# Performance work log

Measured on AMD Instinct MI355X. Metric: run time of the kernel, lower is better.

Reference implementation:

```python
import jax, jax.numpy as jnp
import numpy as np

HEADS = 16
HIDDEN = 1024
DH = HIDDEN // HEADS
EPS = 1e-6


def setup_inputs() -> dict:
    key = jax.random.key(0)
    ks = jax.random.split(key, 18)
    B, S, D, H = 8, 4096, HIDDEN, HEADS
    std = 0.02
    inp = {
        "x": jax.random.normal(ks[0], (B, S, D), dtype=jnp.float32),
        "mask": jnp.zeros((B, 1, S), dtype=jnp.float32),
        "Wq": std * jax.random.normal(ks[1], (D, D), dtype=jnp.float32),
        "bq": jnp.zeros((D,), jnp.float32),
        "Wk": std * jax.random.normal(ks[2], (D, D), dtype=jnp.float32),
        "bk": jnp.zeros((D,), jnp.float32),
        "Wv": std * jax.random.normal(ks[3], (D, D), dtype=jnp.float32),
        "bv": jnp.zeros((D,), jnp.float32),
        "Wa": std * jax.random.normal(ks[4], (D, H), dtype=jnp.float32),
        "ba": jnp.zeros((H,), jnp.float32),
        "Wb": std * jax.random.normal(ks[5], (D, H), dtype=jnp.float32),
        "bb": jnp.zeros((H,), jnp.float32),
        "Wu": std * jax.random.normal(ks[6], (D, D), dtype=jnp.float32),
        "bu": jnp.zeros((D,), jnp.float32),
        "Wo": std * jax.random.normal(ks[7], (D, D), dtype=jnp.float32),
        "bo": jnp.zeros((D,), jnp.float32),
        "ln_g": jnp.ones((D,), jnp.float32),
        "ln_b": jnp.zeros((D,), jnp.float32),
    }
    return inp


def reference(x, mask, Wq, bq, Wk, bk, Wv, bv, Wa, ba, Wb, bb, Wu, bu, Wo, bo, ln_g, ln_b):
    B, S, D = x.shape
    H, dh = HEADS, D // HEADS
    scale = (D / H) ** -0.5

    q = x @ Wq + bq  # [B,S,D]
    k = x @ Wk + bk
    v = x @ Wv + bv

    # alpha pooling of q
    ascore = jnp.swapaxes((q @ Wa + ba) * scale, 1, 2) + mask  # [B,H,S]
    aw = jax.nn.softmax(ascore, axis=-1)
    qh = q.reshape(B, S, H, dh)
    q_av = jnp.einsum("bhs,bshd->bhd", aw, qh).reshape(B, 1, D)  # global query

    p = k * q_av  # [B,S,D], broadcast over seq

    # beta pooling of p
    bscore = jnp.swapaxes((p @ Wb + bb) * scale, 1, 2) + mask  # [B,H,S]
    bw = jax.nn.softmax(bscore, axis=-1)
    ph = p.reshape(B, S, H, dh)
    p_av = jnp.einsum("bhs,bshd->bhd", bw, ph).reshape(B, 1, D)  # global key

    u = p_av * v  # [B,S,D]
    r = u @ Wu + bu
    attn_out = (r + q) @ Wo + bo

    y = x + attn_out  # residual (dropout is identity at inference)
    mu = jnp.mean(y, axis=-1, keepdims=True)
    var = jnp.mean(jnp.square(y - mu), axis=-1, keepdims=True)
    return (y - mu) * jax.lax.rsqrt(var + EPS) * ln_g + ln_b
```

## Files before the change

### kernel.cpp

```cpp
#include <hip/hip_runtime.h>

typedef unsigned short u16;
typedef __bf16 bf16x8 __attribute__((ext_vector_type(8)));
typedef float  f32x4  __attribute__((ext_vector_type(4)));

__device__ __forceinline__ float b2f(u16 u) {
    unsigned int v = ((unsigned int)u) << 16;
    return __builtin_bit_cast(float, v);
}
__device__ __forceinline__ u16 f2b(float f) {
    unsigned int v = __builtin_bit_cast(unsigned int, f);
    v += 0x7fffu + ((v >> 16) & 1u);
    return (u16)(v >> 16);
}

#define GLD16(gp, lp) __builtin_amdgcn_global_load_lds( \
    (const __attribute__((address_space(1))) void*)(gp), \
    (__attribute__((address_space(3))) void*)(lp), 16, 0, 0)


__global__ __launch_bounds__(256) void convert_x(const float* __restrict__ x,
                                                 u16* __restrict__ xb) {
    size_t i = ((size_t)blockIdx.x * 256 + threadIdx.x) * 8;
    float4 v0 = *(const float4*)(x + i);
    float4 v1 = *(const float4*)(x + i + 4);
    ushort4 o0, o1;
    o0.x = f2b(v0.x); o0.y = f2b(v0.y); o0.z = f2b(v0.z); o0.w = f2b(v0.w);
    o1.x = f2b(v1.x); o1.y = f2b(v1.y); o1.z = f2b(v1.z); o1.w = f2b(v1.w);
    *(ushort4*)(xb + i)     = o0;
    *(ushort4*)(xb + i + 4) = o1;
}

__global__ __launch_bounds__(256) void transpose_w(const float* __restrict__ W,
                                                   u16* __restrict__ Wt) {
    __shared__ float tile[64][65];
    int kt = (blockIdx.x & 15) * 64;
    int nt = (blockIdx.x >> 4) * 64;
    int tid = threadIdx.x;
    int r = tid >> 4, c4 = (tid & 15) * 4;
    #pragma unroll
    for (int p = 0; p < 4; ++p) {
        int k = kt + p * 16 + r;
        float4 v = *(const float4*)(W + (size_t)k * 1024 + nt + c4);
        tile[c4 + 0][p * 16 + r] = v.x;
        tile[c4 + 1][p * 16 + r] = v.y;
        tile[c4 + 2][p * 16 + r] = v.z;
        tile[c4 + 3][p * 16 + r] = v.w;
    }
    __syncthreads();
    #pragma unroll
    for (int p = 0; p < 4; ++p) {
        int nl = p * 16 + r;
        ushort4 o;
        o.x = f2b(tile[nl][c4 + 0]); o.y = f2b(tile[nl][c4 + 1]);
        o.z = f2b(tile[nl][c4 + 2]); o.w = f2b(tile[nl][c4 + 3]);
        *(ushort4*)(Wt + (size_t)(nt + nl) * 1024 + kt + c4) = o;
    }
}

__global__ __launch_bounds__(256) void wu_prime(const float* __restrict__ Wu,
                                                const float* __restrict__ p_av,
                                                u16* __restrict__ Wut) {
    __shared__ float tile[64][65];
    int kt = (blockIdx.x & 15) * 64;
    int nt = (blockIdx.x >> 4) * 64;
    int tid = threadIdx.x;
    int r = tid >> 4, c4 = (tid & 15) * 4;
    #pragma unroll
    for (int p = 0; p < 4; ++p) {
        int k = kt + p * 16 + r;
        float4 v = *(const float4*)(Wu + (size_t)k * 1024 + nt + c4);
        tile[c4 + 0][p * 16 + r] = v.x;
        tile[c4 + 1][p * 16 + r] = v.y;
        tile[c4 + 2][p * 16 + r] = v.z;
        tile[c4 + 3][p * 16 + r] = v.w;
    }
    __syncthreads();
    for (int b = 0; b < 8; ++b) {
        float4 pv = *(const float4*)(p_av + (size_t)b * 1024 + kt + c4);
        #pragma unroll
        for (int p = 0; p < 4; ++p) {
            int nl = p * 16 + r;
            ushort4 o;
            o.x = f2b(tile[nl][c4 + 0] * pv.x);
            o.y = f2b(tile[nl][c4 + 1] * pv.y);
            o.z = f2b(tile[nl][c4 + 2] * pv.z);
            o.w = f2b(tile[nl][c4 + 3] * pv.w);
            *(ushort4*)(Wut + ((size_t)b * 1024 + nt + nl) * 1024 + kt + c4) = o;
        }
    }
}

__global__ __launch_bounds__(256) void wat_prep(const float* __restrict__ Wa,
                                                u16* __restrict__ Wat) {
    int idx = blockIdx.x * 256 + threadIdx.x;
    int h = idx >> 10, k = idx & 1023;
    Wat[idx] = f2b(Wa[(k << 4) + h]);
}

__global__ __launch_bounds__(256) void wbt_prep(const float* __restrict__ Wb,
                                                const float* __restrict__ q_av,
                                                u16* __restrict__ Wbt) {
    int idx = blockIdx.x * 256 + threadIdx.x;
    int b = idx >> 14, rem = idx & 16383;
    int h = rem >> 10, k = rem & 1023;
    Wbt[idx] = f2b(Wb[(k << 4) + h] * q_av[(b << 10) + k]);
}

__global__ __launch_bounds__(256) void bias_concat(const float* __restrict__ bq,
                                                   const float* __restrict__ bk,
                                                   const float* __restrict__ bv,
                                                   float* __restrict__ outb) {
    int i = blockIdx.x * 256 + threadIdx.x;
    outb[i] = (i < 1024) ? bq[i] : (i < 2048 ? bk[i - 1024] : bv[i - 2048]);
}

__global__ __launch_bounds__(512, 2)
void gemm_bf16(const u16* __restrict__ A, int lda,
               const u16* __restrict__ Bt,
               const float* __restrict__ bias,
               const u16* __restrict__ addsrc, int ldadd,
               u16* __restrict__ C, int ldc,
               int N, int K, int batch_rows) {
    __shared__ u16 lds[3 * 16384];
    int ntiles = N >> 8;
    int bid = blockIdx.x;
    int mtiles = gridDim.x / ntiles;
    int tm, tn;
    if ((mtiles & 7) == 0) {
        int xcd = bid & 7, s = bid >> 3;
        int mper = mtiles >> 3;
        tm = xcd * mper + s / ntiles;
        tn = s - (s / ntiles) * ntiles;
    } else {
        tm = bid / ntiles; tn = bid - (bid / ntiles) * ntiles;
    }
    int m0 = tm << 8, n0 = tn << 8;
    if (batch_rows > 0) Bt += (size_t)(m0 / batch_rows) * (size_t)N * K;
    int tid = threadIdx.x, lane = tid & 63, w = tid >> 6;
    int wm = w >> 2, wn = w & 3;
    int quad = lane >> 4, l16 = lane & 15;

    int srow = (w << 5) + (lane >> 2);
    int sk = ((lane & 3) ^ ((lane >> 3) & 3)) << 3;
    const u16* Asrc = A  + (size_t)(m0 + srow) * lda + sk;
    const u16* Bsrc = Bt + (size_t)(n0 + srow) * K   + sk;
    int ldst = w << 10;
    int astep = lda << 4, bstep = K << 4;

    int swz = (quad ^ ((l16 >> 1) & 3)) << 3;
    int aoff = (((wm << 7) + l16) << 5) + swz;
    int boff = (((wn << 6) + l16) << 5) + swz + 8192;
    int nt = K >> 5;

    f32x4 zero = {0.f, 0.f, 0.f, 0.f};
    f32x4 acc[8][4];
    #pragma unroll
    for (int i = 0; i < 8; ++i)
        #pragma unroll
        for (int j = 0; j < 4; ++j) acc[i][j] = zero;

    GLD16(Asrc,                &lds[ldst]);
    GLD16(Asrc + astep,        &lds[ldst + 512]);
    GLD16(Bsrc,                &lds[8192 + ldst]);
    GLD16(Bsrc + bstep,        &lds[8192 + ldst + 512]);
    GLD16(Asrc + 32,           &lds[16384 + ldst]);
    GLD16(Asrc + astep + 32,   &lds[16384 + ldst + 512]);
    GLD16(Bsrc + 32,           &lds[16384 + 8192 + ldst]);
    GLD16(Bsrc + bstep + 32,   &lds[16384 + 8192 + ldst + 512]);
    asm volatile("s_waitcnt vmcnt(4)" ::: "memory");
    __builtin_amdgcn_s_barrier();

    int bufc = 0;
    int koff = 64;
    for (int t = 0; t < nt; ++t) {
        const u16* Lc = lds + (bufc << 14);
        int bufs = bufc + 2; if (bufs >= 3) bufs -= 3;
        u16* Ls = lds + (bufs << 14);
        bool pf = (t + 2 < nt);

        bf16x8 bfr[4], afr[4];
        #pragma unroll
        for (int ni = 0; ni < 4; ++ni)
            bfr[ni] = *(const bf16x8*)&Lc[boff + (ni << 9)];
        #pragma unroll
        for (int mi = 0; mi < 4; ++mi)
            afr[mi] = *(const bf16x8*)&Lc[aoff + (mi << 9)];
        if (pf) {
            GLD16(Asrc + koff,         &Ls[ldst]);
            GLD16(Asrc + astep + koff, &Ls[ldst + 512]);
        }
        asm volatile("" ::: "memory");
        __builtin_amdgcn_s_barrier();
        __builtin_amdgcn_s_setprio(1);
        #pragma unroll
        for (int mi = 0; mi < 4; ++mi)
            #pragma unroll
            for (int ni = 0; ni < 4; ++ni)
                acc[mi][ni] = __builtin_amdgcn_mfma_f32_16x16x32_bf16(
                    afr[mi], bfr[ni], acc[mi][ni], 0, 0, 0);
        __builtin_amdgcn_s_setprio(0);
        asm volatile("" ::: "memory");
        __builtin_amdgcn_s_barrier();

        #pragma unroll
        for (int mi = 0; mi < 4; ++mi)
            afr[mi] = *(const bf16x8*)&Lc[aoff + ((mi + 4) << 9)];
        if (pf) {
            GLD16(Bsrc + koff,         &Ls[8192 + ldst]);
            GLD16(Bsrc + bstep + koff, &Ls[8192 + ldst + 512]);
        }
        asm volatile("" ::: "memory");
        __builtin_amdgcn_s_barrier();
        __builtin_amdgcn_s_setprio(1);
        #pragma unroll
        for (int mi = 0; mi < 4; ++mi)
            #pragma unroll
            for (int ni = 0; ni < 4; ++ni)
                acc[mi + 4][ni] = __builtin_amdgcn_mfma_f32_16x16x32_bf16(
                    afr[mi], bfr[ni], acc[mi + 4][ni], 0, 0, 0);
        __builtin_amdgcn_s_setprio(0);
        if (pf) asm volatile("s_waitcnt vmcnt(4)" ::: "memory");
        else    asm volatile("s_waitcnt vmcnt(0)" ::: "memory");
        __builtin_amdgcn_s_barrier();

        koff += 32;
        bufc = (bufc == 2) ? 0 : bufc + 1;
    }

    #pragma unroll
    for (int mi = 0; mi < 8; ++mi) {
        #pragma unroll
        for (int ni = 0; ni < 4; ++ni) {
            int col = n0 + (wn << 6) + (ni << 4) + l16;
            float bv = bias[col];
            #pragma unroll
            for (int rg = 0; rg < 4; ++rg) {
                int rowg = m0 + (wm << 7) + (mi << 4) + (quad << 2) + rg;
                float vv = acc[mi][ni][rg] + bv;
                if (addsrc) vv += b2f(addsrc[(size_t)rowg * ldadd + col]);
                C[(size_t)rowg * ldc + col] = f2b(vv);
            }
        }
    }
}

__global__ __launch_bounds__(256)
void score_gemm(const u16* __restrict__ A, int lda,
                const u16* __restrict__ Bt,
                const float* __restrict__ bias16,
                const float* __restrict__ mask,
                float* __restrict__ outsc,
                int batched) {
    __shared__ u16 As[256 * 64];
    __shared__ u16 Bs[16 * 64];
    int m0 = blockIdx.x << 8;
    int tid = threadIdx.x, lane = tid & 63, w = tid >> 6;
    int quad = lane >> 4, l16 = lane & 15;
    int rph = l16 & 7;
    int lrow = lane >> 3;
    int lkg  = (lane & 7) ^ lrow;
    const u16* Bb = Bt + (batched ? ((size_t)(m0 >> 12) << 14) : 0);

    int idxA = (m0 + (w << 6) + lrow) * lda + (lkg << 3);
    int stepA = lda << 3;
    int idxB = lrow * 1024 + (lkg << 3);

    f32x4 acc4[4];
    #pragma unroll
    for (int i = 0; i < 4; ++i) acc4[i] = (f32x4){0.f, 0.f, 0.f, 0.f};

    for (int kt = 0; kt < 1024; kt += 64) {
        __syncthreads();
        #pragma unroll
        for (int j = 0; j < 8; ++j) {
            int c = (w << 3) + j;
            GLD16(A + (idxA + j * stepA + kt), &As[c << 9]);
        }
        if (w < 2)
            GLD16(Bb + (idxB + w * 8192 + kt), &Bs[w << 9]);
        __syncthreads();
        #pragma unroll
        for (int kk = 0; kk < 2; ++kk) {
            int kg = (((kk << 2) + quad) ^ rph) << 3;
            bf16x8 b = *(const bf16x8*)&Bs[(l16 << 6) + kg];
            #pragma unroll
            for (int mi = 0; mi < 4; ++mi) {
                bf16x8 a = *(const bf16x8*)&As[(((w << 6) + (mi << 4) + l16) << 6) + kg];
                acc4[mi] = __builtin_amdgcn_mfma_f32_16x16x32_bf16(a, b, acc4[mi], 0, 0, 0);
            }
        }
    }
    int bidx = m0 >> 12;
    float bv = bias16[l16];
    float* orow = outsc + (((size_t)bidx << 4) + l16) * 4096;
    const float* mrow = mask + ((size_t)bidx << 12);
    #pragma unroll
    for (int mi = 0; mi < 4; ++mi) {
        int sbase = (m0 & 4095) + (w << 6) + (mi << 4) + (quad << 2);
        #pragma unroll
        for (int rg = 0; rg < 4; ++rg)
            orow[sbase + rg] = 0.125f * (acc4[mi][rg] + bv) + mrow[sbase + rg];
    }
}

__global__ __launch_bounds__(256)
void pool_kernel(const float* __restrict__ score,
                 const u16* __restrict__ X, int ldx,
                 const float* __restrict__ mulvec,
                 float* __restrict__ outav) {
    __shared__ float wbuf[4096];
    __shared__ float red[4];
    __shared__ float psum[16][64];
    int b = blockIdx.x >> 4, h = blockIdx.x & 15;
    int tid = threadIdx.x, lane = tid & 63, w = tid >> 6;
    const float* srow = score + (((size_t)b << 4) + h) * 4096;
    float mx = -1e30f;
    for (int s = tid; s < 4096; s += 256) mx = fmaxf(mx, srow[s]);
    for (int o = 32; o; o >>= 1) mx = fmaxf(mx, __shfl_xor(mx, o));
    if (lane == 0) red[w] = mx;
    __syncthreads();
    mx = fmaxf(fmaxf(red[0], red[1]), fmaxf(red[2], red[3]));
    __syncthreads();
    float sm = 0.f;
    for (int s = tid; s < 4096; s += 256) {
        float e = __expf(srow[s] - mx);
        wbuf[s] = e;
        sm += e;
    }
    for (int o = 32; o; o >>= 1) sm += __shfl_xor(sm, o);
    if (lane == 0) red[w] = sm;
    __syncthreads();
    float inv = 1.f / (red[0] + red[1] + red[2] + red[3]);
    int dg = (tid & 15) << 2;
    int sc = tid >> 4;
    const u16* base = X + ((size_t)(b << 12)) * ldx + (h << 6) + dg;
    float a0 = 0, a1 = 0, a2 = 0, a3 = 0;
    for (int s = sc << 8; s < (sc << 8) + 256; ++s) {
        float wv = wbuf[s];
        ushort4 uv = *(const ushort4*)(base + (size_t)s * ldx);
        a0 += wv * b2f(uv.x); a1 += wv * b2f(uv.y);
        a2 += wv * b2f(uv.z); a3 += wv * b2f(uv.w);
    }
    psum[sc][dg + 0] = a0; psum[sc][dg + 1] = a1;
    psum[sc][dg + 2] = a2; psum[sc][dg + 3] = a3;
    __syncthreads();
    if (tid < 64) {
        float t = 0.f;
        #pragma unroll
        for (int j = 0; j < 16; ++j) t += psum[j][tid];
        t *= inv;
        if (mulvec) t *= mulvec[((size_t)b << 10) + (h << 6) + tid];
        outav[((size_t)b << 10) + (h << 6) + tid] = t;
    }
}

__global__ __launch_bounds__(256)
void ln_kernel(const u16* __restrict__ Z, const float* __restrict__ g,
               const float* __restrict__ bta, float* __restrict__ outp) {
    __shared__ float rs1[4], rs2[4];
    int row = blockIdx.x, tid = threadIdx.x;
    const u16* zr = Z + ((size_t)row << 10);
    ushort4 uv = *(const ushort4*)(zr + (tid << 2));
    float v0 = b2f(uv.x), v1 = b2f(uv.y), v2 = b2f(uv.z), v3 = b2f(uv.w);
    float s = v0 + v1 + v2 + v3;
    float s2 = v0 * v0 + v1 * v1 + v2 * v2 + v3 * v3;
    for (int o = 32; o; o >>= 1) { s += __shfl_xor(s, o); s2 += __shfl_xor(s2, o); }
    if ((tid & 63) == 0) { rs1[tid >> 6] = s; rs2[tid >> 6] = s2; }
    __syncthreads();
    float S = rs1[0] + rs1[1] + rs1[2] + rs1[3];
    float S2 = rs2[0] + rs2[1] + rs2[2] + rs2[3];
    float mean = S * (1.0f / 1024.0f);
    float var = S2 * (1.0f / 1024.0f) - mean * mean;
    float inv = rsqrtf(var + 1e-6f);
    int c = tid << 2;
    float4 o4;
    o4.x = (v0 - mean) * inv * g[c + 0] + bta[c + 0];
    o4.y = (v1 - mean) * inv * g[c + 1] + bta[c + 1];
    o4.z = (v2 - mean) * inv * g[c + 2] + bta[c + 2];
    o4.w = (v3 - mean) * inv * g[c + 3] + bta[c + 3];
    *(float4*)(outp + ((size_t)row << 10) + c) = o4;
}


extern "C" void kernel_launch(void* const* d_in, const int* in_sizes, int n_in,
                              void* d_out, int out_size, void* d_ws, size_t ws_size,
                              hipStream_t stream) {
    (void)in_sizes; (void)n_in; (void)out_size;
    const float* x    = (const float*)d_in[0];
    const float* mask = (const float*)d_in[1];
    const float* Wq   = (const float*)d_in[2];
    const float* bq   = (const float*)d_in[3];
    const float* Wk   = (const float*)d_in[4];
    const float* bk   = (const float*)d_in[5];
    const float* Wv   = (const float*)d_in[6];
    const float* bv   = (const float*)d_in[7];
    const float* Wa   = (const float*)d_in[8];
    const float* ba   = (const float*)d_in[9];
    const float* Wb   = (const float*)d_in[10];
    const float* bb   = (const float*)d_in[11];
    const float* Wu   = (const float*)d_in[12];
    const float* bu   = (const float*)d_in[13];
    const float* Wo   = (const float*)d_in[14];
    const float* bo   = (const float*)d_in[15];
    const float* ln_g = (const float*)d_in[16];
    const float* ln_b = (const float*)d_in[17];
    float* outp = (float*)d_out;

    char* ws = (char*)d_ws;
    u16*   xb    = (u16*)(ws);
    u16*   qkv   = (u16*)(ws + 67108864);
    u16*   Wqkvt = (u16*)(ws + 268435456);
    u16*   Wot   = (u16*)(ws + 274726912);
    u16*   Wat   = (u16*)(ws + 276824064);
    u16*   Wbt   = (u16*)(ws + 276856832);
    float* score = (float*)(ws + 277118976);
    float* q_av  = (float*)(ws + 279216128);
    float* p_av  = (float*)(ws + 279248896);
    float* biasq = (float*)(ws + 279281664);
    u16*   Wubt  = (u16*)(ws + 279293952);
    if (ws_size < 296071168ULL) return;

    convert_x<<<16384, 256, 0, stream>>>(x, xb);
    transpose_w<<<256, 256, 0, stream>>>(Wq, Wqkvt);
    transpose_w<<<256, 256, 0, stream>>>(Wk, Wqkvt + 1048576);
    transpose_w<<<256, 256, 0, stream>>>(Wv, Wqkvt + 2097152);
    transpose_w<<<256, 256, 0, stream>>>(Wo, Wot);
    wat_prep<<<64, 256, 0, stream>>>(Wa, Wat);
    bias_concat<<<12, 256, 0, stream>>>(bq, bk, bv, biasq);

    gemm_bf16<<<1536, 512, 0, stream>>>(xb, 1024, Wqkvt, biasq,
                                        nullptr, 0, qkv, 3072, 3072, 1024, 0);
    score_gemm<<<128, 256, 0, stream>>>(qkv, 3072, Wat, ba, mask, score, 0);
    pool_kernel<<<128, 256, 0, stream>>>(score, qkv, 3072, nullptr, q_av);
    wbt_prep<<<512, 256, 0, stream>>>(Wb, q_av, Wbt);
    score_gemm<<<128, 256, 0, stream>>>(qkv + 1024, 3072, Wbt, bb, mask, score, 1);
    pool_kernel<<<128, 256, 0, stream>>>(score, qkv + 1024, 3072, q_av, p_av);
    wu_prime<<<256, 256, 0, stream>>>(Wu, p_av, Wubt);
    gemm_bf16<<<512, 512, 0, stream>>>(qkv + 2048, 3072, Wubt, bu,
                                       qkv, 3072, qkv, 3072, 1024, 1024, 4096);
    gemm_bf16<<<512, 512, 0, stream>>>(qkv, 3072, Wot, bo,
                                       xb, 1024, xb, 1024, 1024, 1024, 0);
    ln_kernel<<<32768, 256, 0, stream>>>(xb, ln_g, ln_b, outp);
}
```

Measured before the change: 928.1 us.

## Restructure bf16 GEMM main loop into 4-phase K=64 ping-pong schedule

Rewrites the GEMM inner loop so each iteration covers a K=64 step and uses double-buffered LDS split into A/B halves. The 256x256 tile becomes four 128x128 quadrants, each computed in its own phase, with loads for the next stage spread across the phases. The aim is to overlap global-to-LDS copies with MFMA work more finely and to halve the loop overhead per K. The cost is 128KB of LDS per block, which may drop occupancy below the two blocks per CU the launch bounds ask for, plus more barriers per iteration.

```diff
diff --git a/kernel.cpp b/kernel.cpp
--- a/kernel.cpp
+++ b/kernel.cpp
@@ -122,7 +122,7 @@
                const u16* __restrict__ addsrc, int ldadd,
                u16* __restrict__ C, int ldc,
                int N, int K, int batch_rows) {
-    __shared__ u16 lds[3 * 16384];
+    __shared__ u16 lds[65536];
     int ntiles = N >> 8;
     int bid = blockIdx.x;
     int mtiles = gridDim.x / ntiles;
@@ -141,17 +141,30 @@
     int wm = w >> 2, wn = w & 3;
     int quad = lane >> 4, l16 = lane & 15;
 
-    int srow = (w << 5) + (lane >> 2);
-    int sk = ((lane & 3) ^ ((lane >> 3) & 3)) << 3;
-    const u16* Asrc = A  + (size_t)(m0 + srow) * lda + sk;
-    const u16* Bsrc = Bt + (size_t)(n0 + srow) * K   + sk;
-    int ldst = w << 10;
-    int astep = lda << 4, bstep = K << 4;
-
-    int swz = (quad ^ ((l16 >> 1) & 3)) << 3;
-    int aoff = (((wm << 7) + l16) << 5) + swz;
-    int boff = (((wn << 6) + l16) << 5) + swz + 8192;
-    int nt = K >> 5;
+    int srow  = tid >> 2;
+    int schk  = ((tid & 3) ^ ((tid >> 3) & 3)) << 3;
+    const u16* pAs = A  + (size_t)(m0 + srow) * lda + schk;
+    const u16* pBs = Bt + (size_t)(n0 + srow) * K   + schk;
+    int A128 = lda << 7, B128 = K << 7;
+    int wdst = w << 9;
+
+#define STG_A(bufb, mh, kel) do { \
+    GLD16(pAs + ((mh) ? A128 : 0) + (kel),      &lds[(bufb) + (mh)*8192 + wdst]); \
+    GLD16(pAs + ((mh) ? A128 : 0) + (kel) + 32, &lds[(bufb) + (mh)*8192 + 4096 + wdst]); } while (0)
+#define STG_B(bufb, nh, kel) do { \
+    GLD16(pBs + ((nh) ? B128 : 0) + (kel),      &lds[(bufb) + 16384 + (nh)*8192 + wdst]); \
+    GLD16(pBs + ((nh) ? B128 : 0) + (kel) + 32, &lds[(bufb) + 16384 + (nh)*8192 + 4096 + wdst]); } while (0)
+
+    int physc8 = (quad ^ ((l16 >> 1) & 3)) << 3;
+    int aBase = ((wm << 6) + l16) * 32 + physc8;
+    int bBase = 16384 + ((wn << 5) + l16) * 32 + physc8;
+
+#define RDA(bufb, mh, kk, mi) (*(const bf16x8*)&lds[(bufb) + (mh)*8192 + (kk)*4096 + (mi)*512 + aBase])
+#define RDB(bufb, nh, kk, ni) (*(const bf16x8*)&lds[(bufb) + (nh)*8192 + (kk)*4096 + (ni)*512 + bBase])
+#define MFMA16 __builtin_amdgcn_mfma_f32_16x16x32_bf16
+#define CFENCE asm volatile("" ::: "memory")
+#define LGKM0  do { asm volatile("s_waitcnt lgkmcnt(0)" ::: "memory"); \
+                    __builtin_amdgcn_sched_barrier(0); } while (0)
 
     f32x4 zero = {0.f, 0.f, 0.f, 0.f};
     f32x4 acc[8][4];
@@ -160,89 +173,111 @@
         #pragma unroll
         for (int j = 0; j < 4; ++j) acc[i][j] = zero;
 
-    GLD16(Asrc,                &lds[ldst]);
-    GLD16(Asrc + astep,        &lds[ldst + 512]);
-    GLD16(Bsrc,                &lds[8192 + ldst]);
-    GLD16(Bsrc + bstep,        &lds[8192 + ldst + 512]);
-    GLD16(Asrc + 32,           &lds[16384 + ldst]);
-    GLD16(Asrc + astep + 32,   &lds[16384 + ldst + 512]);
-    GLD16(Bsrc + 32,           &lds[16384 + 8192 + ldst]);
-    GLD16(Bsrc + bstep + 32,   &lds[16384 + 8192 + ldst + 512]);
+    STG_A(0, 0, 0); STG_A(0, 1, 0); STG_B(0, 0, 0); STG_B(0, 1, 0);
+    STG_B(32768, 0, 64); STG_A(32768, 1, 64);
     asm volatile("s_waitcnt vmcnt(4)" ::: "memory");
     __builtin_amdgcn_s_barrier();
 
-    int bufc = 0;
-    int koff = 64;
+    int nt = K >> 6;
     for (int t = 0; t < nt; ++t) {
-        const u16* Lc = lds + (bufc << 14);
-        int bufs = bufc + 2; if (bufs >= 3) bufs -= 3;
-        u16* Ls = lds + (bufs << 14);
-        bool pf = (t + 2 < nt);
-
-        bf16x8 bfr[4], afr[4];
-        #pragma unroll
-        for (int ni = 0; ni < 4; ++ni)
-            bfr[ni] = *(const bf16x8*)&Lc[boff + (ni << 9)];
-        #pragma unroll
-        for (int mi = 0; mi < 4; ++mi)
-            afr[mi] = *(const bf16x8*)&Lc[aoff + (mi << 9)];
-        if (pf) {
-            GLD16(Asrc + koff,         &Ls[ldst]);
-            GLD16(Asrc + astep + koff, &Ls[ldst + 512]);
-        }
-        asm volatile("" ::: "memory");
+        int bb = (t & 1) << 15;
+        int ob = bb ^ 32768;
+        int k1 = (t + 1) << 6, k2 = (t + 2) << 6;
+        bool s1 = (t + 1) < nt, s2 = (t + 2) < nt;
+        bf16x8 a[4][2], b[2][2];
+
+        #pragma unroll
+        for (int ni = 0; ni < 2; ++ni) { b[ni][0] = RDB(bb, 0, 0, ni); b[ni][1] = RDB(bb, 0, 1, ni); }
+        #pragma unroll
+        for (int mi = 0; mi < 4; ++mi) { a[mi][0] = RDA(bb, 0, 0, mi); a[mi][1] = RDA(bb, 0, 1, mi); }
+        if (s1) { STG_A(ob, 0, k1); STG_B(ob, 1, k1); }
+        CFENCE; __builtin_amdgcn_s_barrier();
+        LGKM0;
+        __builtin_amdgcn_s_setprio(1);
+        #pragma unroll
+        for (int kk = 0; kk < 2; ++kk)
+            #pragma unroll
+            for (int mi = 0; mi < 4; ++mi)
+                #pragma unroll
+                for (int ni = 0; ni < 2; ++ni)
+                    acc[mi][ni] = MFMA16(a[mi][kk], b[ni][kk], acc[mi][ni], 0, 0, 0);
+        __builtin_amdgcn_s_setprio(0);
+        CFENCE; __builtin_amdgcn_s_barrier();
+
+        #pragma unroll
+        for (int mi = 0; mi < 4; ++mi) { a[mi][0] = RDA(bb, 1, 0, mi); a[mi][1] = RDA(bb, 1, 1, mi); }
+        CFENCE; __builtin_amdgcn_s_barrier();
+        LGKM0;
+        __builtin_amdgcn_s_setprio(1);
+        #pragma unroll
+        for (int kk = 0; kk < 2; ++kk)
+            #pragma unroll
+            for (int mi = 0; mi < 4; ++mi)
+                #pragma unroll
+                for (int ni = 0; ni < 2; ++ni)
+                    acc[4 + mi][ni] = MFMA16(a[mi][kk], b[ni][kk], acc[4 + mi][ni], 0, 0, 0);
+        __builtin_amdgcn_s_setprio(0);
+        CFENCE; __builtin_amdgcn_s_barrier();
+
+        #pragma unroll
+        for (int ni = 0; ni < 2; ++ni) { b[ni][0] = RDB(bb, 1, 0, ni); b[ni][1] = RDB(bb, 1, 1, ni); }
+        if (s2) STG_B(bb, 0, k2);
+        CFENCE; __builtin_amdgcn_s_barrier();
+        LGKM0;
+        __builtin_amdgcn_s_setprio(1);
+        #pragma unroll
+        for (int kk = 0; kk < 2; ++kk)
+            #pragma unroll
+            for (int mi = 0; mi < 4; ++mi)
+                #pragma unroll
+                for (int ni = 0; ni < 2; ++ni)
+                    acc[4 + mi][2 + ni] = MFMA16(a[mi][kk], b[ni][kk], acc[4 + mi][2 + ni], 0, 0, 0);
+        __builtin_amdgcn_s_setprio(0);
+        CFENCE; __builtin_amdgcn_s_barrier();
+
+        #pragma unroll
+        for (int mi = 0; mi < 4; ++mi) { a[mi][0] = RDA(bb, 0, 0, mi); a[mi][1] = RDA(bb, 0, 1, mi); }
+        if (s2) STG_A(bb, 1, k2);
+        CFENCE; __builtin_amdgcn_s_barrier();
+        LGKM0;
+        __builtin_amdgcn_s_setprio(1);
+        #pragma unroll
+        for (int kk = 0; kk < 2; ++kk)
+            #pragma unroll
+            for (int mi = 0; mi < 4; ++mi)
+                #pragma unroll
+                for (int ni = 0; ni < 2; ++ni)
+                    acc[mi][2 + ni] = MFMA16(a[mi][kk], b[ni][kk], acc[mi][2 + ni], 0, 0, 0);
+        __builtin_amdgcn_s_setprio(0);
+        if (s2)      asm volatile("s_waitcnt vmcnt(4)" ::: "memory");
+        else if (s1) asm volatile("s_waitcnt vmcnt(0)" ::: "memory");
         __builtin_amdgcn_s_barrier();
-        __builtin_amdgcn_s_setprio(1);
-        #pragma unroll
-        for (int mi = 0; mi < 4; ++mi)
-            #pragma unroll
-            for (int ni = 0; ni < 4; ++ni)
-                acc[mi][ni] = __builtin_amdgcn_mfma_f32_16x16x32_bf16(
-                    afr[mi], bfr[ni], acc[mi][ni], 0, 0, 0);
-        __builtin_amdgcn_s_setprio(0);
-        asm volatile("" ::: "memory");
-        __builtin_amdgcn_s_barrier();
-
-        #pragma unroll
-        for (int mi = 0; mi < 4; ++mi)
-            afr[mi] = *(const bf16x8*)&Lc[aoff + ((mi + 4) << 9)];
-        if (pf) {
-            GLD16(Bsrc + koff,         &Ls[8192 + ldst]);
-            GLD16(Bsrc + bstep + koff, &Ls[8192 + ldst + 512]);
-        }
-        asm volatile("" ::: "memory");
-        __builtin_amdgcn_s_barrier();
-        __builtin_amdgcn_s_setprio(1);
-        #pragma unroll
-        for (int mi = 0; mi < 4; ++mi)
-            #pragma unroll
-            for (int ni = 0; ni < 4; ++ni)
-                acc[mi + 4][ni] = __builtin_amdgcn_mfma_f32_16x16x32_bf16(
-                    afr[mi], bfr[ni], acc[mi + 4][ni], 0, 0, 0);
-        __builtin_amdgcn_s_setprio(0);
-        if (pf) asm volatile("s_waitcnt vmcnt(4)" ::: "memory");
-        else    asm volatile("s_waitcnt vmcnt(0)" ::: "memory");
-        __builtin_amdgcn_s_barrier();
-
-        koff += 32;
-        bufc = (bufc == 2) ? 0 : bufc + 1;
-    }
-
-    #pragma unroll
-    for (int mi = 0; mi < 8; ++mi) {
-        #pragma unroll
-        for (int ni = 0; ni < 4; ++ni) {
-            int col = n0 + (wn << 6) + (ni << 4) + l16;
+    }
+
+    #pragma unroll
+    for (int mi8 = 0; mi8 < 8; ++mi8) {
+        int mh = mi8 >> 2, mi = mi8 & 3;
+        #pragma unroll
+        for (int ni4 = 0; ni4 < 4; ++ni4) {
+            int nh = ni4 >> 1, ni = ni4 & 1;
+            int col = n0 + (nh << 7) + (wn << 5) + (ni << 4) + l16;
             float bv = bias[col];
             #pragma unroll
             for (int rg = 0; rg < 4; ++rg) {
-                int rowg = m0 + (wm << 7) + (mi << 4) + (quad << 2) + rg;
-                float vv = acc[mi][ni][rg] + bv;
+                int rowg = m0 + (mh << 7) + (wm << 6) + (mi << 4) + (quad << 2) + rg;
+                float vv = acc[mi8][ni4][rg] + bv;
                 if (addsrc) vv += b2f(addsrc[(size_t)rowg * ldadd + col]);
                 C[(size_t)rowg * ldc + col] = f2b(vv);
             }
         }
     }
+#undef STG_A
+#undef STG_B
+#undef RDA
+#undef RDB
+#undef MFMA16
+#undef CFENCE
+#undef LGKM0
 }
 
 __global__ __launch_bounds__(256)
```

New measurement: 943.5 us. Within noise of the previous version (+1.7%).
